# Performance work log

Measured on AMD Instinct MI355X. Metric: run time of the kernel, lower is better.

Reference implementation:

```python
import jax, jax.numpy as jnp
import numpy as np

N_HEAD, D_HEAD = 16, 64
D_MODEL = N_HEAD * D_HEAD
QLEN, MLEN, BSZ = 1024, 1024, 4
KLEN = QLEN + MLEN
LN_EPS = 1e-5


def setup_inputs() -> dict:
    key = jax.random.key(0)
    ks = jax.random.split(key, 8)
    w = jax.random.normal(ks[0], (QLEN, BSZ, D_MODEL), jnp.float32)
    r = jax.random.normal(ks[1], (KLEN, D_MODEL), jnp.float32)
    mems = jax.random.normal(ks[2], (MLEN, BSZ, D_MODEL), jnp.float32)
    # causal mask over (qlen, klen): query i may attend keys j <= i + MLEN
    i = jnp.arange(QLEN)[:, None]
    j = jnp.arange(KLEN)[None, :]
    attn_mask = j > (i + MLEN)  # True = masked
    s = 1.0 / np.sqrt(D_MODEL)
    qkv_w = jax.random.normal(ks[3], (3 * D_MODEL, D_MODEL), jnp.float32) * s
    r_net_w = jax.random.normal(ks[4], (D_MODEL, D_MODEL), jnp.float32) * s
    o_w = jax.random.normal(ks[5], (D_MODEL, D_MODEL), jnp.float32) * s
    r_r_bias = jax.random.normal(ks[6], (N_HEAD, D_HEAD), jnp.float32) * 0.02
    r_w_bias = jax.random.normal(ks[7], (N_HEAD, D_HEAD), jnp.float32) * 0.02
    ln_gamma = jnp.ones((D_MODEL,), jnp.float32)
    ln_beta = jnp.zeros((D_MODEL,), jnp.float32)
    return {"w": w, "r": r, "mems": mems, "attn_mask": attn_mask,
            "qkv_w": qkv_w, "r_net_w": r_net_w, "o_w": o_w,
            "r_r_bias": r_r_bias, "r_w_bias": r_w_bias,
            "ln_gamma": ln_gamma, "ln_beta": ln_beta}


def _layer_norm(x, g, b):
    mu = jnp.mean(x, axis=-1, keepdims=True)
    var = jnp.var(x, axis=-1, keepdims=True)
    return (x - mu) * jax.lax.rsqrt(var + LN_EPS) * g + b


def _rel_shift(x):
    # x: [qlen, rlen, bsz, n_head]
    q, rl, b, n = x.shape
    x_pad = jnp.pad(x, ((0, 0), (1, 0), (0, 0), (0, 0)))  # zero row at front of axis 1
    x_pad = x_pad.reshape(rl + 1, q, b, n)
    return x_pad[1:].reshape(q, rl, b, n)


def reference(w, r, mems, attn_mask, qkv_w, r_net_w, o_w, r_r_bias, r_w_bias, ln_gamma, ln_beta):
    qlen, bsz = w.shape[0], w.shape[1]
    cat = jnp.concatenate([mems, w], axis=0)  # [klen, b, d]
    klen = cat.shape[0]
    w_heads = cat @ qkv_w.T  # [klen, b, 3*d]
    r_head_k = (r @ r_net_w.T).reshape(r.shape[0], N_HEAD, D_HEAD)  # [rlen, n, dh]
    w_q, w_k, w_v = jnp.split(w_heads, 3, axis=-1)
    w_q = w_q[-qlen:].reshape(qlen, bsz, N_HEAD, D_HEAD)
    w_k = w_k.reshape(klen, bsz, N_HEAD, D_HEAD)
    w_v = w_v.reshape(klen, bsz, N_HEAD, D_HEAD)

    scale = 1.0 / np.sqrt(D_HEAD)
    AC = jnp.einsum('ibnd,jbnd->ijbn', w_q + r_w_bias, w_k)
    BD = _rel_shift(jnp.einsum('ibnd,jnd->ijbn', w_q + r_r_bias, r_head_k))
    attn_score = (AC + BD) * scale
    attn_score = jnp.where(attn_mask[None, :, :, None].transpose(1, 2, 0, 3), -1e30, attn_score) if False else \
        jnp.where(attn_mask[:, :, None, None], jnp.float32(-1e30), attn_score)
    attn_prob = jax.nn.softmax(attn_score, axis=1)
    attn_vec = jnp.einsum('ijbn,jbnd->ibnd', attn_prob, w_v)
    attn_vec = attn_vec.reshape(qlen, bsz, N_HEAD * D_HEAD)
    attn_out = attn_vec @ o_w.T
    return _layer_norm(w + attn_out, ln_gamma, ln_beta)
```

## Files before the change

### kernel.cpp

```cpp
#include <hip/hip_runtime.h>
#include <hip/hip_bf16.h>

typedef __attribute__((ext_vector_type(8))) short short8;
typedef __attribute__((ext_vector_type(4))) float f32x4;
typedef __hip_bfloat16 bf16;

#define NHEAD 16
#define DHEAD 64
#define DMODEL 1024
#define QLEN 1024
#define MLEN 1024
#define BSZ 4
#define KLEN 2048
#define LOG2E 1.44269504088896f

__device__ __forceinline__ float fast_exp2(float x) {
#if __has_builtin(__builtin_amdgcn_exp2f)
  return __builtin_amdgcn_exp2f(x);
#else
  return exp2f(x);
#endif
}

__device__ __forceinline__ short8 ld8(const bf16* p) { return *(const short8*)p; }
__device__ __forceinline__ void st8(bf16* p, short8 v) { *(short8*)p = v; }
__device__ __forceinline__ f32x4 mfma16(short8 a, short8 b, f32x4 c) {
  return __builtin_amdgcn_mfma_f32_16x16x32_bf16(a, b, c, 0, 0, 0);
}
__device__ __forceinline__ float bfu2f(unsigned short u) {
  unsigned int x = ((unsigned int)u) << 16;
  return __uint_as_float(x);
}
__device__ __forceinline__ unsigned short f2bfu(float f) {
  bf16 t = __float2bfloat16(f);
  return *(unsigned short*)&t;
}
__device__ __forceinline__ unsigned short f2bfu_fast(float f) {
  return (unsigned short)((__float_as_uint(f) + 0x8000u) >> 16);
}
__device__ __forceinline__ bf16 bf16_raw(unsigned short u) {
  bf16 t; *(unsigned short*)&t = u; return t;
}
__device__ __forceinline__ void async16(const bf16* g, bf16* l) {
  __builtin_amdgcn_global_load_lds(
      (const __attribute__((address_space(1))) unsigned int*)g,
      (__attribute__((address_space(3))) unsigned int*)l, 16, 0, 0);
}

#define DPPF(x, ctrl, rm) \
  __int_as_float(__builtin_amdgcn_update_dpp( \
      __float_as_int(x), __float_as_int(x), (ctrl), (rm), 0xF, false))

__global__ void detect_dtype(const unsigned short* wq, int* flag) {
  const int tid = threadIdx.x;
  int cnt = 0;
  #pragma unroll
  for (int j = 0; j < 8; ++j) {
    unsigned short u = wq[2 * (tid * 8 + j)];
    int e = (u >> 7) & 0xFF;
    if (e >= 100 && e <= 134) cnt++;
  }
  #pragma unroll
  for (int o = 32; o > 0; o >>= 1) cnt += __shfl_xor(cnt, o, 64);
  __shared__ int red[4];
  if ((tid & 63) == 0) red[tid >> 6] = cnt;
  __syncthreads();
  if (tid == 0) {
    int total = red[0] + red[1] + red[2] + red[3];
    *flag = (total > 1024) ? 0 : 1;
  }
}

__global__ __launch_bounds__(256) void convert_inputs(
    const void* s0, const void* s1, const void* s2,
    const void* s3, const void* s4, const void* s5,
    bf16* d0, bf16* d1, bf16* d2, bf16* d3, bf16* d4, bf16* d5,
    const int* flag)
{
  const int b = blockIdx.x;
  const void* src; bf16* dst; int lb;
  if (b < 2048)      { src = s0; dst = d0; lb = b; }
  else if (b < 4096) { src = s1; dst = d1; lb = b - 2048; }
  else if (b < 5120) { src = s2; dst = d2; lb = b - 4096; }
  else if (b < 6656) { src = s3; dst = d3; lb = b - 5120; }
  else if (b < 7168) { src = s4; dst = d4; lb = b - 6656; }
  else               { src = s5; dst = d5; lb = b - 7168; }
  const size_t idx = ((size_t)lb * 256 + threadIdx.x) * 8;
  if (*flag) {
    const f32x4* f = (const f32x4*)src;
    f32x4 a = f[idx >> 2];
    f32x4 c = f[(idx >> 2) + 1];
    short8 v;
    v[0] = (short)f2bfu(a[0]); v[1] = (short)f2bfu(a[1]);
    v[2] = (short)f2bfu(a[2]); v[3] = (short)f2bfu(a[3]);
    v[4] = (short)f2bfu(c[0]); v[5] = (short)f2bfu(c[1]);
    v[6] = (short)f2bfu(c[2]); v[7] = (short)f2bfu(c[3]);
    st8(dst + idx, v);
  } else {
    st8(dst + idx, ld8((const bf16*)src + idx));
  }
}

__device__ __forceinline__ void gemm_core64(
    const bf16* const ap[4], const bf16* const bp[4],
    bf16* As, bf16* Bs, int wv, int wm, int wn, int lr, int lg,
    f32x4 acc[4][4])
{
  const int sx = lr & 7;
  for (int k0 = 0; k0 < DMODEL; k0 += 64) {
    #pragma unroll
    for (int p = 0; p < 4; ++p) {
      async16(ap[p] + k0, As + (wv * 32 + p * 8) * 64);
      async16(bp[p] + k0, Bs + (wv * 32 + p * 8) * 64);
    }
    __syncthreads();
    #pragma unroll
    for (int ks = 0; ks < 2; ++ks) {
      const int col = (((ks * 4 + lg) ^ sx) << 3);
      short8 af[4], bfr[4];
      #pragma unroll
      for (int mt = 0; mt < 4; ++mt) af[mt] = ld8(As + (wm * 64 + mt * 16 + lr) * 64 + col);
      #pragma unroll
      for (int nt = 0; nt < 4; ++nt) bfr[nt] = ld8(Bs + (wn * 64 + nt * 16 + lr) * 64 + col);
      #pragma unroll
      for (int mt = 0; mt < 4; ++mt)
        #pragma unroll
        for (int nt = 0; nt < 4; ++nt)
          acc[mt][nt] = mfma16(af[mt], bfr[nt], acc[mt][nt]);
    }
    __syncthreads();
  }
}

__global__ __launch_bounds__(256) void qkv_gemm(
    const bf16* __restrict__ w, const bf16* __restrict__ mems,
    const bf16* __restrict__ qkv_w,
    const bf16* __restrict__ r, const bf16* __restrict__ rnet_w,
    const void* __restrict__ r_w_bias, const void* __restrict__ r_r_bias,
    const int* __restrict__ flag,
    bf16* __restrict__ qac, bf16* __restrict__ qbd,
    bf16* __restrict__ kbuf, bf16* __restrict__ vbuf,
    bf16* __restrict__ rkbuf)
{
  const int id = blockIdx.x;
  int sec, bx, by;
  if (id < 256)       { sec = 0; bx = id >> 5;                    by = 32 + (id & 31); }
  else if (id < 768)  { sec = 1; int t = id - 256;  bx = 8  + (t >> 6); by = t & 63; }
  else if (id < 1280) { sec = 2; int t = id - 768;  bx = 16 + (t >> 6); by = t & 63; }
  else                { sec = 3; int t = id - 1280; bx = 24 + (t >> 4); by = t & 15; }
  __shared__ bf16 sh[16384];
  bf16* As = sh;
  bf16* Bs = sh + 8192;
  const int tid = threadIdx.x;
  const int lane = tid & 63, wv = tid >> 6;
  const int wm = wv >> 1, wn = wv & 1;
  const int lr = lane & 15, lg = lane >> 4;
  const int lr8 = lane >> 3;
  const int ucol = ((lane & 7) ^ lr8) * 8;
  const bf16 *ap[4], *bp[4];
  #pragma unroll
  for (int p = 0; p < 4; ++p) {
    int arow = wv * 32 + p * 8 + lr8;
    if (sec == 3) {
      ap[p] = r + (size_t)(by * 128 + arow) * DMODEL + ucol;
      bp[p] = rnet_w + (size_t)((bx - 24) * 128 + arow) * DMODEL + ucol;
    } else {
      int m = by * 128 + arow;
      int j = m >> 2, b = m & 3;
      ap[p] = ((j < MLEN) ? (mems + ((size_t)(j * BSZ + b)) * DMODEL)
                          : (w + ((size_t)((j - MLEN) * BSZ + b)) * DMODEL)) + ucol;
      bp[p] = qkv_w + (size_t)(bx * 128 + arow) * DMODEL + ucol;
    }
  }
  f32x4 zero = {0.f, 0.f, 0.f, 0.f};
  f32x4 acc[4][4];
  #pragma unroll
  for (int a = 0; a < 4; ++a)
    #pragma unroll
    for (int c2 = 0; c2 < 4; ++c2) acc[a][c2] = zero;
  gemm_core64(ap, bp, As, Bs, wv, wm, wn, lr, lg, acc);

  if (sec == 2) {
    #pragma unroll
    for (int nt = 0; nt < 4; ++nt) {
      int n = wn * 64 + nt * 16 + lr;
      #pragma unroll
      for (int mt = 0; mt < 4; ++mt) {
        int jl = wm * 16 + mt * 4 + lg;
        #pragma unroll
        for (int rr = 0; rr < 4; ++rr) {
          int x = rr * 32 + jl;
          sh[n * 128 + (((x >> 4) ^ (n & 7)) << 4) + (x & 15)] =
              __float2bfloat16(acc[mt][nt][rr]);
        }
      }
    }
    __syncthreads();
    const int grp = lane >> 3, sl = lane & 7;
    const int hbase = (bx - 16) * 2;
    #pragma unroll
    for (int i = 0; i < 16; ++i) {
      int idx = i * 32 + wv * 8 + grp;
      int n = idx >> 2, bb = idx & 3;
      int x0 = bb * 32 + sl * 4;
      ushort4 v4 = *(const ushort4*)(sh + n * 128 + (((x0 >> 4) ^ (n & 7)) << 4) + (x0 & 15));
      int hh = hbase + (n >> 6), dd = n & 63;
      *(ushort4*)(vbuf + ((size_t)(bb * NHEAD + hh) * DHEAD + dd) * KLEN + by * 32 + sl * 4) = v4;
    }
    return;
  }
  if (sec == 3) {
    #pragma unroll
    for (int nt = 0; nt < 4; ++nt) {
      int col = (bx - 24) * 128 + wn * 64 + nt * 16 + lr;
      int h = col >> 6, d = col & 63;
      #pragma unroll
      for (int mt = 0; mt < 4; ++mt) {
        #pragma unroll
        for (int rr = 0; rr < 4; ++rr) {
          int m = by * 128 + wm * 64 + mt * 16 + lg * 4 + rr;
          rkbuf[((size_t)h * KLEN + m) * DHEAD + d] = __float2bfloat16(acc[mt][nt][rr]);
        }
      }
    }
    return;
  }
  const int isf = (sec == 0) ? *flag : 0;
  const float QSC = 0.125f * LOG2E;
  #pragma unroll
  for (int nt = 0; nt < 4; ++nt) {
    int col = bx * 128 + wn * 64 + nt * 16 + lr;
    int nn = col & 1023;
    int h = nn >> 6, d = nn & 63;
    float rwb = 0.f, rrb = 0.f;
    if (sec == 0) {
      if (isf) { rwb = ((const float*)r_w_bias)[nn]; rrb = ((const float*)r_r_bias)[nn]; }
      else { rwb = __bfloat162float(((const bf16*)r_w_bias)[nn]);
             rrb = __bfloat162float(((const bf16*)r_r_bias)[nn]); }
    }
    #pragma unroll
    for (int mt = 0; mt < 4; ++mt) {
      #pragma unroll
      for (int rr = 0; rr < 4; ++rr) {
        int m = by * 128 + wm * 64 + mt * 16 + lg * 4 + rr;
        int j = m >> 2, b = m & 3;
        float v = acc[mt][nt][rr];
        if (sec == 0) {
          int i = j - MLEN;
          size_t base = (((size_t)(b * NHEAD + h)) * QLEN + i) * DHEAD + d;
          qac[base] = __float2bfloat16((v + rwb) * QSC);
          qbd[base] = __float2bfloat16((v + rrb) * QSC);
        } else {
          kbuf[(((size_t)(b * NHEAD + h)) * KLEN + j) * DHEAD + d] = __float2bfloat16(v);
        }
      }
    }
  }
}

#define RRBODY(RR, CTRL) { \
    const int di = g * 4 + RR; \
    float sh[5]; \
    _Pragma("unroll") for (int ct = 0; ct < 5; ++ct) { \
      float y = Gr[ct][RR]; \
      sh[ct] = __int_as_float(__builtin_amdgcn_update_dpp( \
          __float_as_int(y), __float_as_int(y), (CTRL), 0xF, 0xF, false)); \
    } \
    float sv[4]; \
    _Pragma("unroll") for (int jt = 0; jt < 4; ++jt) { \
      float bd = (c > di) ? sh[jt + 1] : sh[jt]; \
      sv[jt] = S[jt][RR] + bd; \
    } \
    if (lastt) { \
      const int ig = i0 + wv * 16 + di; \
      _Pragma("unroll") for (int jt = 0; jt < 4; ++jt) \
        if (j0 + jt * 16 + c > ig + MLEN) sv[jt] = -1e30f; \
    } \
    _Pragma("unroll") for (int jt = 0; jt < 4; ++jt) { \
      float pv = fast_exp2(sv[jt]); \
      ls[RR] += pv; \
      pw[di * 64 + ((((jt * 2) + (c >> 3)) ^ (di & 7)) << 3) + (c & 7)] = \
          bf16_raw(f2bfu_fast(pv)); \
    } \
  }

__global__ __launch_bounds__(256, 4) void attn_kernel(
    const bf16* __restrict__ qac, const bf16* __restrict__ qbd,
    const bf16* __restrict__ kbuf, const bf16* __restrict__ vbuf,
    const bf16* __restrict__ rkbuf, bf16* __restrict__ av)
{
  const int id = blockIdx.x;
  const int qt = 15 - (id >> 6);
  const int bh = id & 63;
  const int b = bh >> 4, h = bh & 15;
  const int i0 = qt * 64;
  __shared__ bf16 Ks[64 * 64];
  __shared__ bf16 Vt[64 * 64];
  __shared__ bf16 Rs[128 * 64];
  __shared__ bf16 Ps[4 * 16 * 64];
  const int tid = threadIdx.x;
  const int wv = tid >> 6, lane = tid & 63;
  const int c = lane & 15, g = lane >> 4;
  const size_t bhb = (size_t)(b * NHEAD + h);
  const int lr8 = lane >> 3;
  const int ucol = ((lane & 7) ^ lr8) * 8;
  const int sw0 = ((0 + g) ^ (c & 7)) * 8;
  const int sw1 = ((4 + g) ^ (c & 7)) * 8;

  short8 qaf[2], qbf[2];
  {
    const size_t qrow = (bhb * QLEN + i0 + wv * 16 + c) * DHEAD;
    #pragma unroll
    for (int ks = 0; ks < 2; ++ks) {
      qaf[ks] = ld8(qac + qrow + ks * 32 + g * 8);
      qbf[ks] = ld8(qbd + qrow + ks * 32 + g * 8);
    }
  }
  f32x4 zero = {0.f, 0.f, 0.f, 0.f};
  f32x4 O[4];
  #pragma unroll
  for (int dt = 0; dt < 4; ++dt) O[dt] = zero;
  float ls[4] = {0.f, 0.f, 0.f, 0.f};

  bf16* pw = Ps + wv * (16 * 64);
  const bf16* kc = Ks + c * 64;
  const bf16* vc = Vt + c * 64;

  const int relb = c + 48 - wv * 16;
  int loSw[2][5];
  #pragma unroll
  for (int ks = 0; ks < 2; ++ks)
    #pragma unroll
    for (int ct = 0; ct < 5; ++ct) {
      int rel = relb + ct * 16;
      loSw[ks][ct] = (rel & 63) * 64 + (ks ? sw1 : sw0);
    }

  const int ntiles = qt + 17;
  const int mlo0 = 960 - i0;
  const bf16* rkh = rkbuf + (size_t)h * KLEN * DHEAD;

  #pragma unroll
  for (int p = 0; p < 2; ++p) {
    int r0 = wv * 16 + p * 8;
    async16(kbuf + (bhb * KLEN + r0 + lr8) * DHEAD + ucol, Ks + r0 * 64);
  }
  #pragma unroll
  for (int p = 0; p < 4; ++p) {
    int rr = wv * 32 + p * 8;
    async16(rkh + (size_t)(mlo0 + rr + lr8) * DHEAD + ucol, Rs + rr * 64);
  }
  #pragma unroll
  for (int p = 0; p < 2; ++p) {
    int r0 = wv * 16 + p * 8;
    async16(vbuf + (bhb * DHEAD + r0 + lr8) * KLEN + ucol, Vt + r0 * 64);
  }

  int b0e = 0, b1e = 4096;

  for (int t = 0; t < ntiles; ++t) {
    const int j0 = t * 64;
    const int m_lo = mlo0 + j0;
    asm volatile("s_waitcnt vmcnt(2)" ::: "memory");
    __builtin_amdgcn_s_barrier();
    __builtin_amdgcn_sched_barrier(0);

    f32x4 S[4], G[5];
    #pragma unroll
    for (int jt = 0; jt < 4; ++jt) S[jt] = zero;
    #pragma unroll
    for (int ct = 0; ct < 5; ++ct) G[ct] = zero;
    const bf16* rb0 = Rs + b0e;
    const bf16* rb1 = Rs + b1e;
    #pragma unroll
    for (int ks = 0; ks < 2; ++ks) {
      const int sw = ks ? sw1 : sw0;
      #pragma unroll
      for (int jt = 0; jt < 4; ++jt)
        S[jt] = mfma16(qaf[ks], ld8(kc + jt * 1024 + sw), S[jt]);
      #pragma unroll
      for (int ct = 0; ct < 5; ++ct)
        G[ct] = mfma16(qbf[ks], ld8((ct > wv ? rb1 : rb0) + loSw[ks][ct]), G[ct]);
    }
    asm volatile("s_waitcnt vmcnt(0) lgkmcnt(0)" ::: "memory");
    __builtin_amdgcn_s_barrier();
    __builtin_amdgcn_sched_barrier(0);
    if (t + 1 < ntiles) {
      const int j1 = j0 + 64;
      #pragma unroll
      for (int p = 0; p < 2; ++p) {
        int r0 = wv * 16 + p * 8;
        async16(kbuf + (bhb * KLEN + j1 + r0 + lr8) * DHEAD + ucol, Ks + r0 * 64);
        async16(rkh + (size_t)(m_lo + 128 + r0 + lr8) * DHEAD + ucol,
                Rs + b0e + r0 * 64);
      }
      __builtin_amdgcn_sched_barrier(0);
    }
    float Gr[5][4];
    #pragma unroll
    for (int ct = 0; ct < 5; ++ct)
      #pragma unroll
      for (int rr = 0; rr < 4; ++rr) {
        float y = G[ct][rr];
        y = DPPF(y, 0x124, 0xA);
        y = DPPF(y, 0x128, 0xC);
        Gr[ct][rr] = y;
      }
    const bool lastt = (t == ntiles - 1);
    RRBODY(0, 0x121)
    RRBODY(1, 0x122)
    RRBODY(2, 0x123)
    RRBODY(3, 0x124)
    #pragma unroll
    for (int ks = 0; ks < 2; ++ks) {
      short8 pf = ld8(pw + c * 64 + (((ks * 4 + g) ^ (c & 7)) << 3));
      const int sw = ks ? sw1 : sw0;
      #pragma unroll
      for (int dt = 0; dt < 4; ++dt)
        O[dt] = mfma16(pf, ld8(vc + dt * 1024 + sw), O[dt]);
    }
    if (t + 1 < ntiles) {
      asm volatile("s_waitcnt lgkmcnt(0)" ::: "memory");
      __builtin_amdgcn_s_barrier();
      __builtin_amdgcn_sched_barrier(0);
      const int j1 = j0 + 64;
      #pragma unroll
      for (int p = 0; p < 2; ++p) {
        int r0 = wv * 16 + p * 8;
        async16(vbuf + (bhb * DHEAD + r0 + lr8) * KLEN + j1 + ucol, Vt + r0 * 64);
      }
    }
    int tb = b0e; b0e = b1e; b1e = tb;
  }
  #pragma unroll
  for (int rr = 0; rr < 4; ++rr) {
    float s = ls[rr];
    s += DPPF(s, 0xB1, 0xF);
    s += DPPF(s, 0x4E, 0xF);
    s += DPPF(s, 0x141, 0xF);
    s += DPPF(s, 0x140, 0xF);
    ls[rr] = s;
  }
  #pragma unroll
  for (int rr = 0; rr < 4; ++rr) {
    float inv = 1.0f / ls[rr];
    #pragma unroll
    for (int dt = 0; dt < 4; ++dt) {
      int ig = i0 + wv * 16 + g * 4 + rr;
      int d = dt * 16 + c;
      av[((size_t)ig * BSZ + b) * DMODEL + h * DHEAD + d] =
          __float2bfloat16(O[dt][rr] * inv);
    }
  }
}

__global__ __launch_bounds__(256) void out_gemm(
    const bf16* __restrict__ av, const bf16* __restrict__ o_w,
    bf16* __restrict__ ao)
{
  const int id = blockIdx.x;
  const int bx = id >> 5, by = id & 31;
  __shared__ bf16 As[128 * 64];
  __shared__ bf16 Bs[128 * 64];
  const int tid = threadIdx.x;
  const int lane = tid & 63, wv = tid >> 6;
  const int wm = wv >> 1, wn = wv & 1;
  const int lr = lane & 15, lg = lane >> 4;
  const int lr8 = lane >> 3;
  const int ucol = ((lane & 7) ^ lr8) * 8;
  const bf16 *ap[4], *bp[4];
  #pragma unroll
  for (int p = 0; p < 4; ++p) {
    int arow = wv * 32 + p * 8 + lr8;
    ap[p] = av + (size_t)(by * 128 + arow) * DMODEL + ucol;
    bp[p] = o_w + (size_t)(bx * 128 + arow) * DMODEL + ucol;
  }
  f32x4 zero = {0.f, 0.f, 0.f, 0.f};
  f32x4 acc[4][4];
  #pragma unroll
  for (int a = 0; a < 4; ++a)
    #pragma unroll
    for (int c2 = 0; c2 < 4; ++c2) acc[a][c2] = zero;
  gemm_core64(ap, bp, As, Bs, wv, wm, wn, lr, lg, acc);
  #pragma unroll
  for (int nt = 0; nt < 4; ++nt) {
    int col = bx * 128 + wn * 64 + nt * 16 + lr;
    #pragma unroll
    for (int mt = 0; mt < 4; ++mt) {
      #pragma unroll
      for (int rr = 0; rr < 4; ++rr) {
        int m = by * 128 + wm * 64 + mt * 16 + lg * 4 + rr;
        ao[(size_t)m * DMODEL + col] = __float2bfloat16(acc[mt][nt][rr]);
      }
    }
  }
}

__global__ __launch_bounds__(256) void ln_kernel(
    const void* __restrict__ wz, const bf16* __restrict__ ao,
    const void* __restrict__ gz, const void* __restrict__ bz,
    void* __restrict__ outz, const int* __restrict__ flag)
{
  const int m = blockIdx.x;
  const int tid = threadIdx.x;
  const int isf = *flag;
  ushort4 au = ((const ushort4*)ao)[m * 256 + tid];
  float a4[4];
  a4[0] = bfu2f(au.x); a4[1] = bfu2f(au.y); a4[2] = bfu2f(au.z); a4[3] = bfu2f(au.w);
  float x[4], gg[4], bb[4];
  if (isf) {
    f32x4 w4 = ((const f32x4*)wz)[m * 256 + tid];
    f32x4 g4 = ((const f32x4*)gz)[tid];
    f32x4 b4 = ((const f32x4*)bz)[tid];
    #pragma unroll
    for (int k = 0; k < 4; ++k) { x[k] = w4[k] + a4[k]; gg[k] = g4[k]; bb[k] = b4[k]; }
  } else {
    ushort4 w4 = ((const ushort4*)wz)[m * 256 + tid];
    ushort4 g4 = ((const ushort4*)gz)[tid];
    ushort4 b4 = ((const ushort4*)bz)[tid];
    x[0] = bfu2f(w4.x) + a4[0]; x[1] = bfu2f(w4.y) + a4[1];
    x[2] = bfu2f(w4.z) + a4[2]; x[3] = bfu2f(w4.w) + a4[3];
    gg[0] = bfu2f(g4.x); gg[1] = bfu2f(g4.y); gg[2] = bfu2f(g4.z); gg[3] = bfu2f(g4.w);
    bb[0] = bfu2f(b4.x); bb[1] = bfu2f(b4.y); bb[2] = bfu2f(b4.z); bb[3] = bfu2f(b4.w);
  }
  float s = x[0] + x[1] + x[2] + x[3];
  float s2 = x[0]*x[0] + x[1]*x[1] + x[2]*x[2] + x[3]*x[3];
  #pragma unroll
  for (int o = 32; o > 0; o >>= 1) {
    s += __shfl_xor(s, o, 64);
    s2 += __shfl_xor(s2, o, 64);
  }
  __shared__ float red[8];
  const int wv = tid >> 6, lane = tid & 63;
  if (lane == 0) { red[wv] = s; red[4 + wv] = s2; }
  __syncthreads();
  s = red[0] + red[1] + red[2] + red[3];
  s2 = red[4] + red[5] + red[6] + red[7];
  const float mu = s * (1.0f / DMODEL);
  const float var = s2 * (1.0f / DMODEL) - mu * mu;
  const float rstd = rsqrtf(var + 1e-5f);
  float y[4];
  #pragma unroll
  for (int k = 0; k < 4; ++k) y[k] = (x[k] - mu) * rstd * gg[k] + bb[k];
  if (isf) {
    f32x4 o4; o4[0] = y[0]; o4[1] = y[1]; o4[2] = y[2]; o4[3] = y[3];
    ((f32x4*)outz)[m * 256 + tid] = o4;
  } else {
    ushort4 o4;
    o4.x = f2bfu(y[0]); o4.y = f2bfu(y[1]); o4.z = f2bfu(y[2]); o4.w = f2bfu(y[3]);
    ((ushort4*)outz)[m * 256 + tid] = o4;
  }
}

extern "C" void kernel_launch(void* const* d_in, const int* in_sizes, int n_in,
                              void* d_out, int out_size, void* d_ws, size_t ws_size,
                              hipStream_t stream) {
  (void)in_sizes; (void)n_in; (void)out_size; (void)ws_size;
  const void* w      = d_in[0];
  const void* r      = d_in[1];
  const void* mems   = d_in[2];
  const void* qkv_w  = d_in[4];
  const void* rnet_w = d_in[5];
  const void* o_w    = d_in[6];
  const void* rrb    = d_in[7];
  const void* rwb    = d_in[8];
  const void* ln_g   = d_in[9];
  const void* ln_b   = d_in[10];

  char* ws = (char*)d_ws;
  const size_t MB = 1ull << 20;
  bf16* cw    = (bf16*)(ws + 0 * MB);
  bf16* cmems = (bf16*)(ws + 8 * MB);
  bf16* cr    = (bf16*)(ws + 16 * MB);
  bf16* cqkvw = (bf16*)(ws + 20 * MB);
  bf16* crnet = (bf16*)(ws + 26 * MB);
  bf16* cow   = (bf16*)(ws + 28 * MB);
  int*  flag  = (int*)(ws + 30 * MB);
  bf16* qac   = (bf16*)(ws + 31 * MB);
  bf16* qbd   = (bf16*)(ws + 39 * MB);
  bf16* kbuf  = (bf16*)(ws + 47 * MB);
  bf16* vbuf  = (bf16*)(ws + 63 * MB);
  bf16* rkbuf = (bf16*)(ws + 79 * MB);
  bf16* av    = (bf16*)(ws + 83 * MB);
  bf16* ao    = (bf16*)(ws + 0 * MB);

  detect_dtype<<<1, 256, 0, stream>>>((const unsigned short*)w, flag);
  convert_inputs<<<7680, 256, 0, stream>>>(w, mems, r, qkv_w, rnet_w, o_w,
                                           cw, cmems, cr, cqkvw, crnet, cow, flag);
  qkv_gemm<<<1408, 256, 0, stream>>>(cw, cmems, cqkvw, cr, crnet,
                                     rwb, rrb, flag,
                                     qac, qbd, kbuf, vbuf, rkbuf);
  attn_kernel<<<1024, 256, 0, stream>>>(qac, qbd, kbuf, vbuf, rkbuf, av);
  out_gemm<<<256, 256, 0, stream>>>(av, cow, ao);
  ln_kernel<<<dim3(4096), 256, 0, stream>>>(w, ao, ln_g, ln_b, d_out, flag);
}
```

Before: 289.9 us.

## Double query rows per attention block to reuse K/V/R tiles across two subtiles

```diff
diff --git a/kernel.cpp b/kernel.cpp
--- a/kernel.cpp
+++ b/kernel.cpp
@@ -258,46 +258,55 @@
   }
 }
 
-#define RRBODY(RR, CTRL) { \
+#define GROT(Gx) \
+    _Pragma("unroll") for (int ct = 0; ct < 5; ++ct) \
+      _Pragma("unroll") for (int rr = 0; rr < 4; ++rr) { \
+        float y = Gx[ct][rr]; \
+        y = DPPF(y, 0x124, 0xA);            \
+        y = DPPF(y, 0x128, 0xC);            \
+        Gx[ct][rr] = y; \
+      }
+
+#define RRBODY(RR, CTRL, Sx, Gx, lsx, pwx, igb) { \
     const int di = g * 4 + RR; \
     float sh[5]; \
     _Pragma("unroll") for (int ct = 0; ct < 5; ++ct) { \
-      float y = Gr[ct][RR]; \
+      float y = Gx[ct][RR]; \
       sh[ct] = __int_as_float(__builtin_amdgcn_update_dpp( \
           __float_as_int(y), __float_as_int(y), (CTRL), 0xF, 0xF, false)); \
     } \
     float sv[4]; \
     _Pragma("unroll") for (int jt = 0; jt < 4; ++jt) { \
       float bd = (c > di) ? sh[jt + 1] : sh[jt]; \
-      sv[jt] = S[jt][RR] + bd; \
+      sv[jt] = Sx[jt][RR] + bd; \
     } \
-    if (lastt) { \
-      const int ig = i0 + wv * 16 + di; \
+    if (maskt) { \
+      const int ig = (igb) + di; \
       _Pragma("unroll") for (int jt = 0; jt < 4; ++jt) \
         if (j0 + jt * 16 + c > ig + MLEN) sv[jt] = -1e30f; \
     } \
     _Pragma("unroll") for (int jt = 0; jt < 4; ++jt) { \
       float pv = fast_exp2(sv[jt]); \
-      ls[RR] += pv; \
-      pw[di * 64 + ((((jt * 2) + (c >> 3)) ^ (di & 7)) << 3) + (c & 7)] = \
+      lsx[RR] += pv; \
+      pwx[di * 64 + ((((jt * 2) + (c >> 3)) ^ (di & 7)) << 3) + (c & 7)] = \
           bf16_raw(f2bfu_fast(pv)); \
     } \
   }
 
-__global__ __launch_bounds__(256, 4) void attn_kernel(
+__global__ __launch_bounds__(256, 2) void attn_kernel(
     const bf16* __restrict__ qac, const bf16* __restrict__ qbd,
     const bf16* __restrict__ kbuf, const bf16* __restrict__ vbuf,
     const bf16* __restrict__ rkbuf, bf16* __restrict__ av)
 {
   const int id = blockIdx.x;
-  const int qt = 15 - (id >> 6);
+  const int qt = 7 - (id >> 6);
   const int bh = id & 63;
   const int b = bh >> 4, h = bh & 15;
-  const int i0 = qt * 64;
+  const int i0 = qt * 128;
   __shared__ bf16 Ks[64 * 64];
   __shared__ bf16 Vt[64 * 64];
-  __shared__ bf16 Rs[128 * 64];
-  __shared__ bf16 Ps[4 * 16 * 64];
+  __shared__ bf16 Rs[192 * 64];
+  __shared__ bf16 Ps[8 * 16 * 64];
   const int tid = threadIdx.x;
   const int wv = tid >> 6, lane = tid & 63;
   const int c = lane & 15, g = lane >> 4;
@@ -307,37 +316,37 @@
   const int sw0 = ((0 + g) ^ (c & 7)) * 8;
   const int sw1 = ((4 + g) ^ (c & 7)) * 8;
 
-  short8 qaf[2], qbf[2];
+  short8 qaf0[2], qaf1[2], qbf0[2], qbf1[2];
   {
-    const size_t qrow = (bhb * QLEN + i0 + wv * 16 + c) * DHEAD;
+    const size_t qr0 = (bhb * QLEN + i0 + wv * 32 + c) * DHEAD;
+    const size_t qr1 = qr0 + 16 * DHEAD;
     #pragma unroll
     for (int ks = 0; ks < 2; ++ks) {
-      qaf[ks] = ld8(qac + qrow + ks * 32 + g * 8);
-      qbf[ks] = ld8(qbd + qrow + ks * 32 + g * 8);
+      qaf0[ks] = ld8(qac + qr0 + ks * 32 + g * 8);
+      qbf0[ks] = ld8(qbd + qr0 + ks * 32 + g * 8);
+      qaf1[ks] = ld8(qac + qr1 + ks * 32 + g * 8);
+      qbf1[ks] = ld8(qbd + qr1 + ks * 32 + g * 8);
     }
   }
   f32x4 zero = {0.f, 0.f, 0.f, 0.f};
-  f32x4 O[4];
-  #pragma unroll
-  for (int dt = 0; dt < 4; ++dt) O[dt] = zero;
-  float ls[4] = {0.f, 0.f, 0.f, 0.f};
-
-  bf16* pw = Ps + wv * (16 * 64);
+  f32x4 O0[4], O1[4];
+  #pragma unroll
+  for (int dt = 0; dt < 4; ++dt) { O0[dt] = zero; O1[dt] = zero; }
+  float ls0[4] = {0.f, 0.f, 0.f, 0.f};
+  float ls1[4] = {0.f, 0.f, 0.f, 0.f};
+
+  bf16* pw0 = Ps + (wv * 2 + 0) * 1024;
+  bf16* pw1 = Ps + (wv * 2 + 1) * 1024;
   const bf16* kc = Ks + c * 64;
   const bf16* vc = Vt + c * 64;
 
-  const int relb = c + 48 - wv * 16;
-  int loSw[2][5];
-  #pragma unroll
-  for (int ks = 0; ks < 2; ++ks)
-    #pragma unroll
-    for (int ct = 0; ct < 5; ++ct) {
-      int rel = relb + ct * 16;
-      loSw[ks][ct] = (rel & 63) * 64 + (ks ? sw1 : sw0);
-    }
-
-  const int ntiles = qt + 17;
-  const int mlo0 = 960 - i0;
+  const int ofs0 = 112 - wv * 32;
+  const int ofs1 = ofs0 - 16;
+  const int igb0 = i0 + wv * 32;
+  const int igb1 = igb0 + 16;
+
+  const int ntiles = 2 * qt + 18;
+  const int wlo0 = 896 - i0;
   const bf16* rkh = rkbuf + (size_t)h * KLEN * DHEAD;
 
   #pragma unroll
@@ -346,9 +355,9 @@
     async16(kbuf + (bhb * KLEN + r0 + lr8) * DHEAD + ucol, Ks + r0 * 64);
   }
   #pragma unroll
-  for (int p = 0; p < 4; ++p) {
-    int rr = wv * 32 + p * 8;
-    async16(rkh + (size_t)(mlo0 + rr + lr8) * DHEAD + ucol, Rs + rr * 64);
+  for (int p = 0; p < 6; ++p) {
+    int r0 = wv * 48 + p * 8;
+    async16(rkh + (size_t)(wlo0 + r0 + lr8) * DHEAD + ucol, Rs + r0 * 64);
   }
   #pragma unroll
   for (int p = 0; p < 2; ++p) {
@@ -356,68 +365,97 @@
     async16(vbuf + (bhb * DHEAD + r0 + lr8) * KLEN + ucol, Vt + r0 * 64);
   }
 
-  int b0e = 0, b1e = 4096;
+  const bf16 *rb0 = Rs, *rb1 = Rs + 4096, *rb2 = Rs + 8192;
 
   for (int t = 0; t < ntiles; ++t) {
     const int j0 = t * 64;
-    const int m_lo = mlo0 + j0;
-    asm volatile("s_waitcnt vmcnt(2)" ::: "memory");
+    const bool maskt = (t >= ntiles - 2);
+    if (t + 1 < ntiles) {
+      asm volatile("s_waitcnt vmcnt(2)" ::: "memory");
+    } else {
+      asm volatile("s_waitcnt vmcnt(0)" ::: "memory");
+    }
     __builtin_amdgcn_s_barrier();
     __builtin_amdgcn_sched_barrier(0);
 
-    f32x4 S[4], G[5];
-    #pragma unroll
-    for (int jt = 0; jt < 4; ++jt) S[jt] = zero;
-    #pragma unroll
-    for (int ct = 0; ct < 5; ++ct) G[ct] = zero;
-    const bf16* rb0 = Rs + b0e;
-    const bf16* rb1 = Rs + b1e;
+    f32x4 S0[4], S1[4];
+    #pragma unroll
+    for (int jt = 0; jt < 4; ++jt) { S0[jt] = zero; S1[jt] = zero; }
     #pragma unroll
     for (int ks = 0; ks < 2; ++ks) {
       const int sw = ks ? sw1 : sw0;
       #pragma unroll
-      for (int jt = 0; jt < 4; ++jt)
-        S[jt] = mfma16(qaf[ks], ld8(kc + jt * 1024 + sw), S[jt]);
-      #pragma unroll
-      for (int ct = 0; ct < 5; ++ct)
-        G[ct] = mfma16(qbf[ks], ld8((ct > wv ? rb1 : rb0) + loSw[ks][ct]), G[ct]);
+      for (int jt = 0; jt < 4; ++jt) {
+        short8 kf = ld8(kc + jt * 1024 + sw);
+        S0[jt] = mfma16(qaf0[ks], kf, S0[jt]);
+        S1[jt] = mfma16(qaf1[ks], kf, S1[jt]);
+      }
+    }
+    f32x4 G0[5];
+    #pragma unroll
+    for (int ct = 0; ct < 5; ++ct) G0[ct] = zero;
+    #pragma unroll
+    for (int ks = 0; ks < 2; ++ks) {
+      const int sw = ks ? sw1 : sw0;
+      #pragma unroll
+      for (int ct = 0; ct < 5; ++ct) {
+        int rel = ofs0 + 16 * ct;
+        int qq = rel >> 6;
+        const bf16* rp = (qq == 0) ? rb0 : ((qq == 1) ? rb1 : rb2);
+        G0[ct] = mfma16(qbf0[ks], ld8(rp + (c + (rel & 63)) * 64 + sw), G0[ct]);
+      }
+    }
+    GROT(G0)
+    RRBODY(0, 0x121, S0, G0, ls0, pw0, igb0)
+    RRBODY(1, 0x122, S0, G0, ls0, pw0, igb0)
+    RRBODY(2, 0x123, S0, G0, ls0, pw0, igb0)
+    RRBODY(3, 0x124, S0, G0, ls0, pw0, igb0)
+    f32x4 G1[5];
+    #pragma unroll
+    for (int ct = 0; ct < 5; ++ct) G1[ct] = zero;
+    #pragma unroll
+    for (int ks = 0; ks < 2; ++ks) {
+      const int sw = ks ? sw1 : sw0;
+      #pragma unroll
+      for (int ct = 0; ct < 5; ++ct) {
+        int rel = ofs1 + 16 * ct;
+        int qq = rel >> 6;
+        const bf16* rp = (qq == 0) ? rb0 : ((qq == 1) ? rb1 : rb2);
+        G1[ct] = mfma16(qbf1[ks], ld8(rp + (c + (rel & 63)) * 64 + sw), G1[ct]);
+      }
     }
     asm volatile("s_waitcnt vmcnt(0) lgkmcnt(0)" ::: "memory");
     __builtin_amdgcn_s_barrier();
     __builtin_amdgcn_sched_barrier(0);
     if (t + 1 < ntiles) {
       const int j1 = j0 + 64;
+      const int snew = wlo0 + 192 + j0;
       #pragma unroll
       for (int p = 0; p < 2; ++p) {
         int r0 = wv * 16 + p * 8;
         async16(kbuf + (bhb * KLEN + j1 + r0 + lr8) * DHEAD + ucol, Ks + r0 * 64);
-        async16(rkh + (size_t)(m_lo + 128 + r0 + lr8) * DHEAD + ucol,
-                Rs + b0e + r0 * 64);
+        async16(rkh + (size_t)(snew + r0 + lr8) * DHEAD + ucol,
+                (bf16*)rb0 + r0 * 64);
       }
       __builtin_amdgcn_sched_barrier(0);
     }
-    float Gr[5][4];
-    #pragma unroll
-    for (int ct = 0; ct < 5; ++ct)
-      #pragma unroll
-      for (int rr = 0; rr < 4; ++rr) {
-        float y = G[ct][rr];
-        y = DPPF(y, 0x124, 0xA);
-        y = DPPF(y, 0x128, 0xC);
-        Gr[ct][rr] = y;
-      }
-    const bool lastt = (t == ntiles - 1);
-    RRBODY(0, 0x121)
-    RRBODY(1, 0x122)
-    RRBODY(2, 0x123)
-    RRBODY(3, 0x124)
+    GROT(G1)
+    RRBODY(0, 0x121, S1, G1, ls1, pw1, igb1)
+    RRBODY(1, 0x122, S1, G1, ls1, pw1, igb1)
+    RRBODY(2, 0x123, S1, G1, ls1, pw1, igb1)
+    RRBODY(3, 0x124, S1, G1, ls1, pw1, igb1)
     #pragma unroll
     for (int ks = 0; ks < 2; ++ks) {
-      short8 pf = ld8(pw + c * 64 + (((ks * 4 + g) ^ (c & 7)) << 3));
+      const int psw = (((ks * 4 + g) ^ (c & 7)) << 3);
+      short8 pf0 = ld8(pw0 + c * 64 + psw);
+      short8 pf1 = ld8(pw1 + c * 64 + psw);
       const int sw = ks ? sw1 : sw0;
       #pragma unroll
-      for (int dt = 0; dt < 4; ++dt)
-        O[dt] = mfma16(pf, ld8(vc + dt * 1024 + sw), O[dt]);
+      for (int dt = 0; dt < 4; ++dt) {
+        short8 vf = ld8(vc + dt * 1024 + sw);
+        O0[dt] = mfma16(pf0, vf, O0[dt]);
+        O1[dt] = mfma16(pf1, vf, O1[dt]);
+      }
     }
     if (t + 1 < ntiles) {
       asm volatile("s_waitcnt lgkmcnt(0)" ::: "memory");
@@ -430,26 +468,36 @@
         async16(vbuf + (bhb * DHEAD + r0 + lr8) * KLEN + j1 + ucol, Vt + r0 * 64);
       }
     }
-    int tb = b0e; b0e = b1e; b1e = tb;
+    const bf16* tb = rb0; rb0 = rb1; rb1 = rb2; rb2 = tb;
   }
   #pragma unroll
   for (int rr = 0; rr < 4; ++rr) {
-    float s = ls[rr];
+    float s = ls0[rr];
     s += DPPF(s, 0xB1, 0xF);
     s += DPPF(s, 0x4E, 0xF);
     s += DPPF(s, 0x141, 0xF);
     s += DPPF(s, 0x140, 0xF);
-    ls[rr] = s;
+    ls0[rr] = s;
+    float s1 = ls1[rr];
+    s1 += DPPF(s1, 0xB1, 0xF);
+    s1 += DPPF(s1, 0x4E, 0xF);
+    s1 += DPPF(s1, 0x141, 0xF);
+    s1 += DPPF(s1, 0x140, 0xF);
+    ls1[rr] = s1;
   }
   #pragma unroll
   for (int rr = 0; rr < 4; ++rr) {
-    float inv = 1.0f / ls[rr];
+    float inv0 = 1.0f / ls0[rr];
+    float inv1 = 1.0f / ls1[rr];
     #pragma unroll
     for (int dt = 0; dt < 4; ++dt) {
-      int ig = i0 + wv * 16 + g * 4 + rr;
       int d = dt * 16 + c;
-      av[((size_t)ig * BSZ + b) * DMODEL + h * DHEAD + d] =
-          __float2bfloat16(O[dt][rr] * inv);
+      int ig0 = igb0 + g * 4 + rr;
+      int ig1 = igb1 + g * 4 + rr;
+      av[((size_t)ig0 * BSZ + b) * DMODEL + h * DHEAD + d] =
+          __float2bfloat16(O0[dt][rr] * inv0);
+      av[((size_t)ig1 * BSZ + b) * DMODEL + h * DHEAD + d] =
+          __float2bfloat16(O1[dt][rr] * inv1);
     }
   }
 }
@@ -590,7 +638,7 @@
   qkv_gemm<<<1408, 256, 0, stream>>>(cw, cmems, cqkvw, cr, crnet,
                                      rwb, rrb, flag,
                                      qac, qbd, kbuf, vbuf, rkbuf);
-  attn_kernel<<<1024, 256, 0, stream>>>(qac, qbd, kbuf, vbuf, rkbuf, av);
+  attn_kernel<<<512, 256, 0, stream>>>(qac, qbd, kbuf, vbuf, rkbuf, av);
   out_gemm<<<256, 256, 0, stream>>>(av, cow, ao);
   ln_kernel<<<dim3(4096), 256, 0, stream>>>(w, ao, ln_g, ln_b, d_out, flag);
 }
```

Result: no change. 293.7 us (+1.3%).
